# Kernel optimization log

Hardware: AMD Instinct MI355X
Metric: run time of the kernel (lower is better)

Reference implementation:

```python
import jax, jax.numpy as jnp
import numpy as np

N_NODES, N_EDGES, F_IN, HID, N_CLASSES = 50000, 800000, 128, 128, 10
HEADS, D_HEAD, N_GRAPHS, N_CONV = 4, 32, 256, 3
BN_EPS = 1e-5
NEG_SLOPE = 0.2


def batchnorm(x, g, b):
    # training-mode BN: batch mean / biased variance over dim 0
    m = x.mean(axis=0)
    v = x.var(axis=0)
    return (x - m) * jax.lax.rsqrt(v + BN_EPS) * g + b


def segment_softmax(logits, seg, n):
    # numerically stable softmax over edges grouped by destination node
    m = jax.ops.segment_max(logits, seg, num_segments=n)
    e = jnp.exp(logits - m[seg])
    s = jax.ops.segment_sum(e, seg, num_segments=n)
    return e / (s[seg] + 1e-16)


def gat_conv(x, src, dst, W, a_src, a_dst, bias):
    # PyG GATConv (concat=True), eval mode (no attention dropout)
    n = x.shape[0]
    h = (x @ W).reshape(n, HEADS, D_HEAD)                 # [N,H,Dh]
    al_s = jnp.einsum('nhd,hd->nh', h, a_src)             # alpha from source
    al_d = jnp.einsum('nhd,hd->nh', h, a_dst)             # alpha from dest
    logits = jax.nn.leaky_relu(al_s[src] + al_d[dst], NEG_SLOPE)   # [E,H]
    alpha = segment_softmax(logits, dst, n)                # softmax over incoming edges
    msg = h[src] * alpha[:, :, None]                       # [E,H,Dh]
    out = jax.ops.segment_sum(msg, dst, num_segments=n)    # [N,H,Dh]
    return out.reshape(n, HEADS * D_HEAD) + bias


def setup_inputs() -> dict:
    key = jax.random.key(0)
    ks = jax.random.split(key, 12)
    s = 0.05
    inp = {
        'x': jax.random.normal(ks[0], (N_NODES, F_IN), dtype=jnp.float32),
        'edge_index': jax.random.randint(ks[1], (2, N_EDGES), 0, N_NODES, dtype=jnp.int32),
        'batch': jnp.sort(jax.random.randint(ks[2], (N_NODES,), 0, N_GRAPHS, dtype=jnp.int32)),
        # GCNConv(gfn=True): plain weight, no bias used
        'w_feat': s * jax.random.normal(ks[3], (F_IN, HID), dtype=jnp.float32),
        'bnf_g': jnp.ones((F_IN,), jnp.float32),
        'bnf_b': jnp.full((F_IN,), 1e-4, jnp.float32),
        'bnc_g': jnp.ones((N_CONV, HID), jnp.float32),
        'bnc_b': jnp.full((N_CONV, HID), 1e-4, jnp.float32),
        'gat_w': s * jax.random.normal(ks[4], (N_CONV, HID, HID), dtype=jnp.float32),
        'gat_asrc': s * jax.random.normal(ks[5], (N_CONV, HEADS, D_HEAD), dtype=jnp.float32),
        'gat_adst': s * jax.random.normal(ks[6], (N_CONV, HEADS, D_HEAD), dtype=jnp.float32),
        'gat_b': jnp.zeros((N_CONV, HID), jnp.float32),
        'bnfc_g': jnp.ones((HID,), jnp.float32),
        'bnfc_b': jnp.full((HID,), 1e-4, jnp.float32),
        'lin_w': s * jax.random.normal(ks[7], (HID, HID), dtype=jnp.float32),
        'lin_b': jnp.zeros((HID,), jnp.float32),
        'bnh_g': jnp.ones((HID,), jnp.float32),
        'bnh_b': jnp.full((HID,), 1e-4, jnp.float32),
        'cls_w': s * jax.random.normal(ks[8], (HID, N_CLASSES), dtype=jnp.float32),
        'cls_b': jnp.zeros((N_CLASSES,), jnp.float32),
    }
    return inp


def reference(x, edge_index, batch, w_feat, bnf_g, bnf_b, bnc_g, bnc_b,
              gat_w, gat_asrc, gat_adst, gat_b, bnfc_g, bnfc_b,
              lin_w, lin_b, bnh_g, bnh_b, cls_w, cls_b):
    n = x.shape[0]
    loops = jnp.arange(n, dtype=edge_index.dtype)
    src = jnp.concatenate([edge_index[0], loops])   # self-loops (PyG GATConv default)
    dst = jnp.concatenate([edge_index[1], loops])

    h = jax.nn.relu(batchnorm(x, bnf_g, bnf_b) @ w_feat)   # bn_feat + gfn GCNConv + relu
    for i in range(N_CONV):
        h = batchnorm(h, bnc_g[i], bnc_b[i])
        h = jax.nn.relu(gat_conv(h, src, dst, gat_w[i], gat_asrc[i], gat_adst[i], gat_b[i]))

    g = jax.ops.segment_sum(h, batch, num_segments=N_GRAPHS)   # global_add_pool [G,HID]
    g = jax.nn.relu(batchnorm(g, bnfc_g, bnfc_b) @ lin_w + lin_b)
    g = batchnorm(g, bnh_g, bnh_b)
    # dropout inactive in eval mode
    return jax.nn.log_softmax(g @ cls_w + cls_b, axis=-1)
```

## Files before the change

kernel.cpp:

```cpp
#include <hip/hip_runtime.h>
#include <math.h>

#define N_NODES 50000
#define N_EDGES 800000
#define NGRAPHS 256
#define NCONV 3
#define SCAT_CHUNK 2048
#define DMAX 64
#define GEMM_BLOCKS 782

typedef _Float16 h4 __attribute__((ext_vector_type(4)));
typedef _Float16 h8 __attribute__((ext_vector_type(8)));
typedef float f32x4 __attribute__((ext_vector_type(4)));

static inline int divup(int a, int b) { return (a + b - 1) / b; }

#define SB_CONV 0
#define SB_H2 2048
#define SB_X 2304
#define SB_TOT 2560

#define NSCAT_BLOCKS 3128

__global__ void init_kernel(float* __restrict__ SB, int* __restrict__ cursor,
                            unsigned short* __restrict__ col, int n) {
    int i = blockIdx.x * blockDim.x + threadIdx.x;
    if (i < SB_TOT) SB[i] = 0.f;
    if (i < n) {
        cursor[i] = 1;
        col[(size_t)i * DMAX] = (unsigned short)i;
    }
}

__global__ __launch_bounds__(256) void cast_stats(const float* __restrict__ x,
                                                  _Float16* __restrict__ y, int n,
                                                  float* __restrict__ sums) {
    __shared__ float S[16][128], S2[16][128];
    int tid = threadIdx.x;
    int c8 = (tid & 15) * 8;
    int rg = tid >> 4;
    float s[8] = {}, s2[8] = {};
    for (int r = blockIdx.x * 16 + rg; r < n; r += gridDim.x * 16) {
        const float4* p = (const float4*)&x[(size_t)r * 128 + c8];
        float4 v0 = p[0], v1 = p[1];
        float f[8] = {v0.x, v0.y, v0.z, v0.w, v1.x, v1.y, v1.z, v1.w};
        h8 o;
#pragma unroll
        for (int i = 0; i < 8; ++i) {
            o[i] = (_Float16)f[i];
            s[i] += f[i];
            s2[i] += f[i] * f[i];
        }
        *(h8*)&y[(size_t)r * 128 + c8] = o;
    }
#pragma unroll
    for (int i = 0; i < 8; ++i) { S[rg][c8 + i] = s[i]; S2[rg][c8 + i] = s2[i]; }
    __syncthreads();
    if (tid < 128) {
        float a = 0.f, b = 0.f;
#pragma unroll
        for (int k = 0; k < 16; ++k) { a += S[k][tid]; b += S2[k][tid]; }
        atomicAdd(&sums[tid], a);
        atomicAdd(&sums[128 + tid], b);
    }
}

__global__ __launch_bounds__(256) void colstats_h(const _Float16* __restrict__ x, int n,
                                                  float* __restrict__ sums) {
    __shared__ float S[16][128], S2[16][128];
    int tid = threadIdx.x;
    int c8 = (tid & 15) * 8;
    int rg = tid >> 4;
    float s[8] = {}, s2[8] = {};
    for (int r = blockIdx.x * 16 + rg; r < n; r += gridDim.x * 16) {
        h8 v = *(const h8*)&x[(size_t)r * 128 + c8];
#pragma unroll
        for (int i = 0; i < 8; ++i) {
            float f = (float)v[i];
            s[i] += f;
            s2[i] += f * f;
        }
    }
#pragma unroll
    for (int i = 0; i < 8; ++i) { S[rg][c8 + i] = s[i]; S2[rg][c8 + i] = s2[i]; }
    __syncthreads();
    if (tid < 128) {
        float a = 0.f, b = 0.f;
#pragma unroll
        for (int k = 0; k < 16; ++k) { a += S[k][tid]; b += S2[k][tid]; }
        atomicAdd(&sums[(blockIdx.x & 7) * 256 + tid], a);
        atomicAdd(&sums[(blockIdx.x & 7) * 256 + 128 + tid], b);
    }
}

__global__ __launch_bounds__(128) void fold_t(const float* __restrict__ sums, int nsl,
                                              float inv_n,
                                              const float* __restrict__ gamma,
                                              const float* __restrict__ beta,
                                              const float* __restrict__ W,
                                              _Float16* __restrict__ WTh, float* __restrict__ bp) {
    int j = blockIdx.x, k = threadIdx.x;
    float s1 = 0.f, s2v = 0.f;
    for (int s = 0; s < nsl; ++s) { s1 += sums[s * 256 + k]; s2v += sums[s * 256 + 128 + k]; }
    float mean = s1 * inv_n;
    float var = s2v * inv_n - mean * mean;
    float sc = gamma[k] * rsqrtf(var + 1e-5f);
    float t = beta[k] - mean * sc;
    float w = W[k * 128 + j];
    WTh[j * 128 + k] = (_Float16)(sc * w);
    float pb = t * w;
    for (int off = 1; off < 64; off <<= 1) pb += __shfl_xor(pb, off, 64);
    __shared__ float r2[2];
    if ((k & 63) == 0) r2[k >> 6] = pb;
    __syncthreads();
    if (k == 0) bp[j] = r2[0] + r2[1];
}

__global__ __launch_bounds__(256) void gemm_mfma(const _Float16* __restrict__ Ah,
                                                 const _Float16* __restrict__ WTh,
                                                 const float* __restrict__ bp,
                                                 _Float16* __restrict__ outh, int n, int relu,
                                                 const float* __restrict__ asrc,
                                                 const float* __restrict__ adst,
                                                 float* __restrict__ als,
                                                 float* __restrict__ ald,
                                                 float* __restrict__ stats8,
                                                 float* __restrict__ sums_zero,
                                                 float* __restrict__ g_zero,
                                                 const int* __restrict__ s_src,
                                                 const int* __restrict__ s_dst,
                                                 int* __restrict__ s_cursor,
                                                 unsigned short* __restrict__ s_col, int s_E) {
    __shared__ _Float16 Wl[128 * 136];
    __shared__ float SSm[4 * 128], SS2m[4 * 128];
    int tid = threadIdx.x;
    if ((int)blockIdx.x >= GEMM_BLOCKS) {
        int sb = blockIdx.x - GEMM_BLOCKS;
        int slice = sb & 7;
        int base = (sb >> 3) * SCAT_CHUNK;
        int lim = min(base + SCAT_CHUNK, s_E);
        int lo = slice * (N_NODES / 8);
        int hi = lo + (N_NODES / 8);
        for (int i = base + tid; i < lim; i += 256) {
            int d = s_dst[i];
            if (d >= lo && d < hi) {
                int p = atomicAdd(&s_cursor[d], 1);
                if (p < DMAX) s_col[(size_t)d * DMAX + p] = (unsigned short)s_src[i];
            }
        }
        return;
    }
    if (sums_zero && blockIdx.x < 8) sums_zero[blockIdx.x * 256 + tid] = 0.f;
    if (g_zero && blockIdx.x < 128) g_zero[blockIdx.x * 256 + tid] = 0.f;
    for (int i = tid; i < 2048; i += 256) {
        int r = i >> 4, s = i & 15;
        *(h8*)&Wl[r * 136 + s * 8] = *(const h8*)&WTh[r * 128 + s * 8];
    }
    __syncthreads();
    int lane = tid & 63, wid = tid >> 6;
    int m = lane & 15, quad = lane >> 4;
    int rbase = blockIdx.x * 64 + wid * 16;
    bool act = rbase < n;
    const bool do_al = (asrc != nullptr);
    const bool do_st = (stats8 != nullptr);
    float st[8] = {}, s2t[8] = {};
    float ps[4][4] = {}, pd[4][4] = {};

    if (act) {
        const _Float16* arow = Ah + (size_t)(rbase + m) * 128 + quad * 8;
        h8 af0 = *(const h8*)(arow);
        h8 af1 = *(const h8*)(arow + 32);
        h8 af2 = *(const h8*)(arow + 64);
        h8 af3 = *(const h8*)(arow + 96);
#pragma unroll
        for (int t = 0; t < 8; ++t) {
            const _Float16* wrow = &Wl[(t * 16 + m) * 136 + quad * 8];
            f32x4 acc = {0.f, 0.f, 0.f, 0.f};
            acc = __builtin_amdgcn_mfma_f32_16x16x32_f16(af0, *(const h8*)(wrow), acc, 0, 0, 0);
            acc = __builtin_amdgcn_mfma_f32_16x16x32_f16(af1, *(const h8*)(wrow + 32), acc, 0, 0, 0);
            acc = __builtin_amdgcn_mfma_f32_16x16x32_f16(af2, *(const h8*)(wrow + 64), acc, 0, 0, 0);
            acc = __builtin_amdgcn_mfma_f32_16x16x32_f16(af3, *(const h8*)(wrow + 96), acc, 0, 0, 0);
            int j = t * 16 + m;
            float bj = bp[j];
            float avs = 0.f, avd = 0.f;
            if (do_al) { avs = asrc[j]; avd = adst[j]; }
            int hh = t >> 1;
#pragma unroll
            for (int r = 0; r < 4; ++r) {
                float o = acc[r] + bj;
                if (do_al) {
                    ps[r][hh] += o * avs;
                    pd[r][hh] += o * avd;
                }
                float v = relu ? fmaxf(o, 0.f) : o;
                _Float16 hv16 = (_Float16)v;
                int row = rbase + quad * 4 + r;
                outh[(size_t)row * 128 + j] = hv16;
                if (do_st) {
                    float fv = (float)hv16;
                    st[t] += fv;
                    s2t[t] += fv * fv;
                }
            }
        }
        if (do_al) {
#pragma unroll
            for (int r = 0; r < 4; ++r) {
#pragma unroll
                for (int hh = 0; hh < 4; ++hh) {
                    float v = ps[r][hh];
                    v += __shfl_xor(v, 1, 64); v += __shfl_xor(v, 2, 64);
                    v += __shfl_xor(v, 4, 64); v += __shfl_xor(v, 8, 64);
                    float w = pd[r][hh];
                    w += __shfl_xor(w, 1, 64); w += __shfl_xor(w, 2, 64);
                    w += __shfl_xor(w, 4, 64); w += __shfl_xor(w, 8, 64);
                    if (m == 0) {
                        int row = rbase + quad * 4 + r;
                        als[row * 4 + hh] = v;
                        ald[row * 4 + hh] = w;
                    }
                }
            }
        }
    }
    if (do_st) {
#pragma unroll
        for (int t = 0; t < 8; ++t) {
            st[t] += __shfl_xor(st[t], 16, 64);  st[t] += __shfl_xor(st[t], 32, 64);
            s2t[t] += __shfl_xor(s2t[t], 16, 64); s2t[t] += __shfl_xor(s2t[t], 32, 64);
        }
        if (quad == 0) {
#pragma unroll
            for (int t = 0; t < 8; ++t) {
                SSm[wid * 128 + t * 16 + m] = st[t];
                SS2m[wid * 128 + t * 16 + m] = s2t[t];
            }
        }
        __syncthreads();
        int c = tid & 127, which = tid >> 7;
        const float* A = which ? SS2m : SSm;
        float tot = A[c] + A[128 + c] + A[256 + c] + A[384 + c];
        atomicAdd(&stats8[(blockIdx.x & 7) * 256 + which * 128 + c], tot);
    }
}

__device__ __forceinline__ float leaky(float x) { return fmaxf(x, 0.2f * x); }

__global__ __launch_bounds__(256) void gat_aggregate(const _Float16* __restrict__ hp,
                                                     const float* __restrict__ al_s,
                                                     const float* __restrict__ al_d,
                                                     const int* __restrict__ cnt_arr,
                                                     const unsigned short* __restrict__ col,
                                                     const float* __restrict__ bias,
                                                     _Float16* __restrict__ h_out, int n) {
    int tid = threadIdx.x;
    int lane = tid & 63, wid = tid >> 6;
    int node = blockIdx.x * 4 + wid;
    int beg = node * DMAX;
    int end = beg + min(cnt_arr[node], DMAX);
    int q = lane >> 4, l4 = lane & 15;
    int head = l4 >> 2;
    int f0 = l4 * 8;
    float adh = al_d[node * 4 + head];
    float ch = leaky(adh);
    const _Float16* hpf = hp + f0;
    int last = end - 1;
    float ws = 0.f;
    float a0 = 0.f, a1 = 0.f, a2 = 0.f, a3 = 0.f, a4 = 0.f, a5 = 0.f, a6 = 0.f, a7 = 0.f;
    for (int e = beg + q; e < end; e += 16) {
        int e1 = e + 4, e2 = e + 8, e3 = e + 12;
        bool v1 = e1 < end, v2 = e2 < end, v3 = e3 < end;
        unsigned s0 = (unsigned)col[e];
        unsigned s1 = (unsigned)col[v1 ? e1 : last];
        unsigned s2 = (unsigned)col[v2 ? e2 : last];
        unsigned s3 = (unsigned)col[v3 ? e3 : last];
        float as0 = al_s[s0 * 4 + head];
        float as1 = al_s[s1 * 4 + head];
        float as2 = al_s[s2 * 4 + head];
        float as3 = al_s[s3 * 4 + head];
        h8 hv0 = *(const h8*)(hpf + (size_t)s0 * 128);
        h8 hv1 = *(const h8*)(hpf + (size_t)s1 * 128);
        h8 hv2 = *(const h8*)(hpf + (size_t)s2 * 128);
        h8 hv3 = *(const h8*)(hpf + (size_t)s3 * 128);
        float w0 = __expf(fminf(leaky(as0 + adh) - ch, 10.f));
        float w1 = v1 ? __expf(fminf(leaky(as1 + adh) - ch, 10.f)) : 0.f;
        float w2 = v2 ? __expf(fminf(leaky(as2 + adh) - ch, 10.f)) : 0.f;
        float w3 = v3 ? __expf(fminf(leaky(as3 + adh) - ch, 10.f)) : 0.f;
        ws += (w0 + w1) + (w2 + w3);
        a0 += (float)hv0[0] * w0 + (float)hv1[0] * w1 + (float)hv2[0] * w2 + (float)hv3[0] * w3;
        a1 += (float)hv0[1] * w0 + (float)hv1[1] * w1 + (float)hv2[1] * w2 + (float)hv3[1] * w3;
        a2 += (float)hv0[2] * w0 + (float)hv1[2] * w1 + (float)hv2[2] * w2 + (float)hv3[2] * w3;
        a3 += (float)hv0[3] * w0 + (float)hv1[3] * w1 + (float)hv2[3] * w2 + (float)hv3[3] * w3;
        a4 += (float)hv0[4] * w0 + (float)hv1[4] * w1 + (float)hv2[4] * w2 + (float)hv3[4] * w3;
        a5 += (float)hv0[5] * w0 + (float)hv1[5] * w1 + (float)hv2[5] * w2 + (float)hv3[5] * w3;
        a6 += (float)hv0[6] * w0 + (float)hv1[6] * w1 + (float)hv2[6] * w2 + (float)hv3[6] * w3;
        a7 += (float)hv0[7] * w0 + (float)hv1[7] * w1 + (float)hv2[7] * w2 + (float)hv3[7] * w3;
    }
#pragma unroll
    for (int off = 16; off <= 32; off <<= 1) {
        ws += __shfl_xor(ws, off, 64);
        a0 += __shfl_xor(a0, off, 64); a1 += __shfl_xor(a1, off, 64);
        a2 += __shfl_xor(a2, off, 64); a3 += __shfl_xor(a3, off, 64);
        a4 += __shfl_xor(a4, off, 64); a5 += __shfl_xor(a5, off, 64);
        a6 += __shfl_xor(a6, off, 64); a7 += __shfl_xor(a7, off, 64);
    }
    if (q == 0) {
        float inv = 1.f / (ws + 1e-16f);
        float4 b0 = *(const float4*)&bias[f0];
        float4 b1 = *(const float4*)&bias[f0 + 4];
        h8 ov;
        ov[0] = (_Float16)fmaxf(a0 * inv + b0.x, 0.f);
        ov[1] = (_Float16)fmaxf(a1 * inv + b0.y, 0.f);
        ov[2] = (_Float16)fmaxf(a2 * inv + b0.z, 0.f);
        ov[3] = (_Float16)fmaxf(a3 * inv + b0.w, 0.f);
        ov[4] = (_Float16)fmaxf(a4 * inv + b1.x, 0.f);
        ov[5] = (_Float16)fmaxf(a5 * inv + b1.y, 0.f);
        ov[6] = (_Float16)fmaxf(a6 * inv + b1.z, 0.f);
        ov[7] = (_Float16)fmaxf(a7 * inv + b1.w, 0.f);
        *(h8*)&h_out[(size_t)node * 128 + f0] = ov;
    }
}

__global__ void pool_kernel(const _Float16* __restrict__ h, const int* __restrict__ batch,
                            float* __restrict__ g, int n, int chunk) {
    int f = threadIdx.x;
    int a = blockIdx.x * chunk;
    if (a >= n) return;
    int b = min(n, a + chunk);
    float acc = 0.f;
    int cur = batch[a];
    for (int i = a; i < b; ++i) {
        int bi = batch[i];
        if (bi != cur) {
            atomicAdd(&g[cur * 128 + f], acc);
            acc = 0.f;
            cur = bi;
        }
        acc += (float)h[(size_t)i * 128 + f];
    }
    atomicAdd(&g[cur * 128 + f], acc);
}

__global__ __launch_bounds__(256) void gemm128_bn(const float* __restrict__ A,
                                                  const float* __restrict__ W,
                                                  const float* __restrict__ bias,
                                                  float inv_n,
                                                  const float* __restrict__ gamma,
                                                  const float* __restrict__ beta,
                                                  float* __restrict__ out,
                                                  float* __restrict__ outstats, int n) {
    __shared__ float Wl[128 * 128];
    __shared__ float hT[128 * 32];
    __shared__ float S[16][128], S2[16][128];
    __shared__ float sS[128], tS[128];
    int tid = threadIdx.x;
    for (int i = tid; i < 4096; i += 256) {
        ((float4*)Wl)[i] = ((const float4*)W)[i];
    }
    {
        int c8 = (tid & 15) * 8;
        int rg = tid >> 4;
        float s[8] = {}, s2[8] = {};
        for (int r = rg; r < n; r += 16) {
            const float4* p = (const float4*)&A[(size_t)r * 128 + c8];
            float4 v0 = p[0], v1 = p[1];
            float f[8] = {v0.x, v0.y, v0.z, v0.w, v1.x, v1.y, v1.z, v1.w};
#pragma unroll
            for (int i = 0; i < 8; ++i) { s[i] += f[i]; s2[i] += f[i] * f[i]; }
        }
#pragma unroll
        for (int i = 0; i < 8; ++i) { S[rg][c8 + i] = s[i]; S2[rg][c8 + i] = s2[i]; }
    }
    __syncthreads();
    if (tid < 128) {
        float a = 0.f, b2 = 0.f;
#pragma unroll
        for (int k = 0; k < 16; ++k) { a += S[k][tid]; b2 += S2[k][tid]; }
        float m = a * inv_n;
        float var = b2 * inv_n - m * m;
        float sc = gamma[tid] * rsqrtf(var + 1e-5f);
        sS[tid] = sc;
        tS[tid] = beta[tid] - m * sc;
    }
    __syncthreads();
    int base = blockIdx.x * 32;
    for (int pass = 0; pass < 4; ++pass) {
        int r = (tid >> 5) + pass * 8;
        int c4 = tid & 31;
        int row = base + r;
        float4 v = (row < n) ? ((const float4*)(A + (size_t)row * 128))[c4]
                             : make_float4(0.f, 0.f, 0.f, 0.f);
        int c0 = c4 * 4;
        hT[(c0 + 0) * 32 + r] = v.x * sS[c0 + 0] + tS[c0 + 0];
        hT[(c0 + 1) * 32 + r] = v.y * sS[c0 + 1] + tS[c0 + 1];
        hT[(c0 + 2) * 32 + r] = v.z * sS[c0 + 2] + tS[c0 + 2];
        hT[(c0 + 3) * 32 + r] = v.w * sS[c0 + 3] + tS[c0 + 3];
    }
    __syncthreads();
    int tx = tid & 31, ty = tid >> 5;
    int j0 = tx * 4, r0 = ty * 4;
    float acc[4][4] = {};
#pragma unroll 8
    for (int k = 0; k < 128; ++k) {
        float4 a = *(const float4*)&hT[k * 32 + r0];
        float4 w = *(const float4*)&Wl[k * 128 + j0];
        acc[0][0] += a.x * w.x; acc[0][1] += a.x * w.y; acc[0][2] += a.x * w.z; acc[0][3] += a.x * w.w;
        acc[1][0] += a.y * w.x; acc[1][1] += a.y * w.y; acc[1][2] += a.y * w.z; acc[1][3] += a.y * w.w;
        acc[2][0] += a.z * w.x; acc[2][1] += a.z * w.y; acc[2][2] += a.z * w.z; acc[2][3] += a.z * w.w;
        acc[3][0] += a.w * w.x; acc[3][1] += a.w * w.y; acc[3][2] += a.w * w.z; acc[3][3] += a.w * w.w;
    }
    float4 bb = *(const float4*)&bias[j0];
    float csum[4] = {}, csq[4] = {};
    for (int i2 = 0; i2 < 4; ++i2) {
        int row = base + r0 + i2;
        if (row < n) {
            float o0 = fmaxf(acc[i2][0] + bb.x, 0.f);
            float o1 = fmaxf(acc[i2][1] + bb.y, 0.f);
            float o2 = fmaxf(acc[i2][2] + bb.z, 0.f);
            float o3 = fmaxf(acc[i2][3] + bb.w, 0.f);
            *(float4*)&out[(size_t)row * 128 + j0] = make_float4(o0, o1, o2, o3);
            csum[0] += o0; csum[1] += o1; csum[2] += o2; csum[3] += o3;
            csq[0] += o0 * o0; csq[1] += o1 * o1; csq[2] += o2 * o2; csq[3] += o3 * o3;
        }
    }
#pragma unroll
    for (int c = 0; c < 4; ++c) {
        atomicAdd(&outstats[j0 + c], csum[c]);
        atomicAdd(&outstats[128 + j0 + c], csq[c]);
    }
}

__global__ __launch_bounds__(64) void final_kernel(const float* __restrict__ g2,
                                                   const float* __restrict__ stats, float inv_n,
                                                   const float* __restrict__ gamma,
                                                   const float* __restrict__ beta,
                                                   const float* __restrict__ W,
                                                   const float* __restrict__ b,
                                                   float* __restrict__ out, int rows) {
    int r = blockIdx.x;
    if (r >= rows) return;
    int lane = threadIdx.x;
    float logit[10] = {};
    for (int k = lane; k < 128; k += 64) {
        float m = stats[k] * inv_n;
        float var = stats[128 + k] * inv_n - m * m;
        float sc = gamma[k] * rsqrtf(var + 1e-5f);
        float gv = (g2[r * 128 + k] - m) * sc + beta[k];
#pragma unroll
        for (int j = 0; j < 10; ++j) logit[j] += gv * W[k * 10 + j];
    }
#pragma unroll
    for (int j = 0; j < 10; ++j)
        for (int off = 1; off < 64; off <<= 1) logit[j] += __shfl_xor(logit[j], off, 64);
    if (lane == 0) {
        float m = -1e30f;
#pragma unroll
        for (int j = 0; j < 10; ++j) { logit[j] += b[j]; m = fmaxf(m, logit[j]); }
        float sum = 0.f;
#pragma unroll
        for (int j = 0; j < 10; ++j) sum += expf(logit[j] - m);
        float lse = m + logf(sum);
#pragma unroll
        for (int j = 0; j < 10; ++j) out[r * 10 + j] = logit[j] - lse;
    }
}

extern "C" void kernel_launch(void* const* d_in, const int* in_sizes, int n_in,
                              void* d_out, int out_size, void* d_ws, size_t ws_size,
                              hipStream_t stream) {
    const float* x      = (const float*)d_in[0];
    const int*   ei     = (const int*)d_in[1];
    const int*   batch  = (const int*)d_in[2];
    const float* w_feat = (const float*)d_in[3];
    const float* bnf_g  = (const float*)d_in[4];
    const float* bnf_b  = (const float*)d_in[5];
    const float* bnc_g  = (const float*)d_in[6];
    const float* bnc_b  = (const float*)d_in[7];
    const float* gat_w  = (const float*)d_in[8];
    const float* gat_as = (const float*)d_in[9];
    const float* gat_ad = (const float*)d_in[10];
    const float* gat_b  = (const float*)d_in[11];
    const float* bnfc_g = (const float*)d_in[12];
    const float* bnfc_b = (const float*)d_in[13];
    const float* lin_w  = (const float*)d_in[14];
    const float* lin_b  = (const float*)d_in[15];
    const float* bnh_g  = (const float*)d_in[16];
    const float* bnh_b  = (const float*)d_in[17];
    const float* cls_w  = (const float*)d_in[18];
    const float* cls_b  = (const float*)d_in[19];
    float* out = (float*)d_out;

    char* ws = (char*)d_ws;
    size_t off = 0;
    auto alloc = [&](size_t bytes) -> void* {
        void* p = ws + off;
        off = (off + bytes + 255) & ~(size_t)255;
        return p;
    };
    _Float16* xh   = (_Float16*)alloc((size_t)N_NODES * 128 * 2);
    _Float16* h    = (_Float16*)alloc((size_t)N_NODES * 128 * 2);
    _Float16* hp   = (_Float16*)alloc((size_t)N_NODES * 128 * 2);
    float*    als  = (float*)alloc((size_t)N_NODES * 4 * 4);
    float*    ald  = (float*)alloc((size_t)N_NODES * 4 * 4);
    int*      curs = (int*)alloc((size_t)N_NODES * 4);
    unsigned short* col = (unsigned short*)alloc((size_t)N_NODES * DMAX * 2);
    float*    SB   = (float*)alloc(SB_TOT * 4);
    _Float16* WTh  = (_Float16*)alloc(128 * 128 * 2);
    float*    bp   = (float*)alloc(128 * 4);
    float*    g    = (float*)alloc(NGRAPHS * 128 * 4);
    float*    g2   = (float*)alloc(NGRAPHS * 128 * 4);

    const int* esrc = ei;
    const int* edst = ei + N_EDGES;

    init_kernel<<<divup(N_NODES, 256), 256, 0, stream>>>(SB, curs, col, N_NODES);

    cast_stats<<<256, 256, 0, stream>>>(x, xh, N_NODES, SB + SB_X);

    fold_t<<<128, 128, 0, stream>>>(SB + SB_X, 1, 1.f / N_NODES, bnf_g, bnf_b, w_feat, WTh, bp);
    gemm_mfma<<<GEMM_BLOCKS + NSCAT_BLOCKS, 256, 0, stream>>>(xh, WTh, bp, h, N_NODES, 1,
                                                      nullptr, nullptr, nullptr, nullptr,
                                                      SB + SB_CONV, nullptr, nullptr,
                                                      esrc, edst, curs, col, N_EDGES);

    for (int i = 0; i < NCONV; ++i) {
        fold_t<<<128, 128, 0, stream>>>(SB + SB_CONV, 8, 1.f / N_NODES,
                                        bnc_g + 128 * i, bnc_b + 128 * i,
                                        gat_w + 16384 * i, WTh, bp);
        gemm_mfma<<<GEMM_BLOCKS, 256, 0, stream>>>(h, WTh, bp, hp, N_NODES, 0,
                                                   gat_as + 128 * i, gat_ad + 128 * i,
                                                   als, ald, nullptr, SB + SB_CONV,
                                                   (i == 2) ? g : nullptr,
                                                   nullptr, nullptr, nullptr, nullptr, 0);
        gat_aggregate<<<N_NODES / 4, 256, 0, stream>>>(hp, als, ald, curs, col,
                                                       gat_b + 128 * i, h, N_NODES);
        if (i < NCONV - 1)
            colstats_h<<<256, 256, 0, stream>>>(h, N_NODES, SB + SB_CONV);
    }

    pool_kernel<<<divup(N_NODES, 32), 128, 0, stream>>>(h, batch, g, N_NODES, 32);
    gemm128_bn<<<divup(NGRAPHS, 32), 256, 0, stream>>>(g, lin_w, lin_b, 1.f / NGRAPHS,
                                                       bnfc_g, bnfc_b, g2, SB + SB_H2, NGRAPHS);
    final_kernel<<<NGRAPHS, 64, 0, stream>>>(g2, SB + SB_H2, 1.f / NGRAPHS, bnh_g, bnh_b,
                                             cls_w, cls_b, out, NGRAPHS);
}
```

Baseline: 376.4 us.

## Split edge-scatter CSR build across two GEMMs and use 512-thread GEMM blocks

The edge bucketing (CSR column fill) that was fused entirely into the first GEMM launch is now split into two halves: the first half runs alongside the feature GEMM and the second alongside the first GAT GEMM, with bigger 4096-edge chunks. GEMM blocks grow to 512 threads covering 128 rows each, halving the block count, and per-block column stats are reduced through shared-memory atomics instead of a per-wave array. The aim is to spread the scatter work so it hides behind two GEMMs and to cut the launch/W-staging overhead per row. The cost is more LDS atomics and possibly lower occupancy from the larger blocks.

After: 373.3 us. Within noise of the previous version (-0.8%).

```diff
diff --git a/kernel.cpp b/kernel.cpp
--- a/kernel.cpp
+++ b/kernel.cpp
@@ -5,9 +5,11 @@
 #define N_EDGES 800000
 #define NGRAPHS 256
 #define NCONV 3
-#define SCAT_CHUNK 2048
 #define DMAX 64
-#define GEMM_BLOCKS 782
+#define GEMM_BLOCKS 391
+#define SCHUNK 4096
+#define NCHUNKS 196
+#define HALF0 98
 
 typedef _Float16 h4 __attribute__((ext_vector_type(4)));
 typedef _Float16 h8 __attribute__((ext_vector_type(8)));
@@ -19,8 +21,6 @@
 #define SB_H2 2048
 #define SB_X 2304
 #define SB_TOT 2560
-
-#define NSCAT_BLOCKS 3128
 
 __global__ void init_kernel(float* __restrict__ SB, int* __restrict__ cursor,
                             unsigned short* __restrict__ col, int n) {
@@ -116,7 +116,7 @@
     if (k == 0) bp[j] = r2[0] + r2[1];
 }
 
-__global__ __launch_bounds__(256) void gemm_mfma(const _Float16* __restrict__ Ah,
+__global__ __launch_bounds__(512) void gemm_mfma(const _Float16* __restrict__ Ah,
                                                  const _Float16* __restrict__ WTh,
                                                  const float* __restrict__ bp,
                                                  _Float16* __restrict__ outh, int n, int relu,
@@ -130,18 +130,20 @@
                                                  const int* __restrict__ s_src,
                                                  const int* __restrict__ s_dst,
                                                  int* __restrict__ s_cursor,
-                                                 unsigned short* __restrict__ s_col, int s_E) {
+                                                 unsigned short* __restrict__ s_col,
+                                                 int s_E, int s_chunk0) {
     __shared__ _Float16 Wl[128 * 136];
-    __shared__ float SSm[4 * 128], SS2m[4 * 128];
+    __shared__ float Sl2[256];
     int tid = threadIdx.x;
     if ((int)blockIdx.x >= GEMM_BLOCKS) {
         int sb = blockIdx.x - GEMM_BLOCKS;
         int slice = sb & 7;
-        int base = (sb >> 3) * SCAT_CHUNK;
-        int lim = min(base + SCAT_CHUNK, s_E);
+        int chunk = s_chunk0 + (sb >> 3);
+        int base = chunk * SCHUNK;
+        int lim = min(base + SCHUNK, s_E);
         int lo = slice * (N_NODES / 8);
         int hi = lo + (N_NODES / 8);
-        for (int i = base + tid; i < lim; i += 256) {
+        for (int i = base + tid; i < lim; i += 512) {
             int d = s_dst[i];
             if (d >= lo && d < hi) {
                 int p = atomicAdd(&s_cursor[d], 1);
@@ -150,19 +152,20 @@
         }
         return;
     }
-    if (sums_zero && blockIdx.x < 8) sums_zero[blockIdx.x * 256 + tid] = 0.f;
-    if (g_zero && blockIdx.x < 128) g_zero[blockIdx.x * 256 + tid] = 0.f;
-    for (int i = tid; i < 2048; i += 256) {
+    if (sums_zero && blockIdx.x < 4) sums_zero[blockIdx.x * 512 + tid] = 0.f;
+    if (g_zero && blockIdx.x < 64) g_zero[blockIdx.x * 512 + tid] = 0.f;
+    const bool do_st = (stats8 != nullptr);
+    if (do_st && tid < 256) Sl2[tid] = 0.f;
+    for (int i = tid; i < 2048; i += 512) {
         int r = i >> 4, s = i & 15;
         *(h8*)&Wl[r * 136 + s * 8] = *(const h8*)&WTh[r * 128 + s * 8];
     }
     __syncthreads();
     int lane = tid & 63, wid = tid >> 6;
     int m = lane & 15, quad = lane >> 4;
-    int rbase = blockIdx.x * 64 + wid * 16;
+    int rbase = blockIdx.x * 128 + wid * 16;
     bool act = rbase < n;
     const bool do_al = (asrc != nullptr);
-    const bool do_st = (stats8 != nullptr);
     float st[8] = {}, s2t[8] = {};
     float ps[4][4] = {}, pd[4][4] = {};
 
@@ -229,18 +232,15 @@
             st[t] += __shfl_xor(st[t], 16, 64);  st[t] += __shfl_xor(st[t], 32, 64);
             s2t[t] += __shfl_xor(s2t[t], 16, 64); s2t[t] += __shfl_xor(s2t[t], 32, 64);
         }
-        if (quad == 0) {
+        if (quad == 0 && act) {
 #pragma unroll
             for (int t = 0; t < 8; ++t) {
-                SSm[wid * 128 + t * 16 + m] = st[t];
-                SS2m[wid * 128 + t * 16 + m] = s2t[t];
+                atomicAdd(&Sl2[t * 16 + m], st[t]);
+                atomicAdd(&Sl2[128 + t * 16 + m], s2t[t]);
             }
         }
         __syncthreads();
-        int c = tid & 127, which = tid >> 7;
-        const float* A = which ? SS2m : SSm;
-        float tot = A[c] + A[128 + c] + A[256 + c] + A[384 + c];
-        atomicAdd(&stats8[(blockIdx.x & 7) * 256 + which * 128 + c], tot);
+        if (tid < 256) atomicAdd(&stats8[(blockIdx.x & 7) * 256 + tid], Sl2[tid]);
     }
 }
 
@@ -518,20 +518,25 @@
     cast_stats<<<256, 256, 0, stream>>>(x, xh, N_NODES, SB + SB_X);
 
     fold_t<<<128, 128, 0, stream>>>(SB + SB_X, 1, 1.f / N_NODES, bnf_g, bnf_b, w_feat, WTh, bp);
-    gemm_mfma<<<GEMM_BLOCKS + NSCAT_BLOCKS, 256, 0, stream>>>(xh, WTh, bp, h, N_NODES, 1,
-                                                      nullptr, nullptr, nullptr, nullptr,
-                                                      SB + SB_CONV, nullptr, nullptr,
-                                                      esrc, edst, curs, col, N_EDGES);
+    gemm_mfma<<<GEMM_BLOCKS + HALF0 * 8, 512, 0, stream>>>(
+        xh, WTh, bp, h, N_NODES, 1,
+        nullptr, nullptr, nullptr, nullptr,
+        SB + SB_CONV, nullptr, nullptr,
+        esrc, edst, curs, col, N_EDGES, 0);
 
     for (int i = 0; i < NCONV; ++i) {
         fold_t<<<128, 128, 0, stream>>>(SB + SB_CONV, 8, 1.f / N_NODES,
                                         bnc_g + 128 * i, bnc_b + 128 * i,
                                         gat_w + 16384 * i, WTh, bp);
-        gemm_mfma<<<GEMM_BLOCKS, 256, 0, stream>>>(h, WTh, bp, hp, N_NODES, 0,
-                                                   gat_as + 128 * i, gat_ad + 128 * i,
-                                                   als, ald, nullptr, SB + SB_CONV,
-                                                   (i == 2) ? g : nullptr,
-                                                   nullptr, nullptr, nullptr, nullptr, 0);
+        int nblk = GEMM_BLOCKS + ((i == 0) ? (NCHUNKS - HALF0) * 8 : 0);
+        gemm_mfma<<<nblk, 512, 0, stream>>>(
+            h, WTh, bp, hp, N_NODES, 0,
+            gat_as + 128 * i, gat_ad + 128 * i,
+            als, ald, nullptr, SB + SB_CONV,
+            (i == 2) ? g : nullptr,
+            (i == 0) ? esrc : nullptr, (i == 0) ? edst : nullptr,
+            (i == 0) ? curs : nullptr, (i == 0) ? col : nullptr,
+            (i == 0) ? N_EDGES : 0, HALF0);
         gat_aggregate<<<N_NODES / 4, 256, 0, stream>>>(hp, als, ald, curs, col,
                                                        gat_b + 128 * i, h, N_NODES);
         if (i < NCONV - 1)
```
